# Kernel optimization log

Hardware: AMD Instinct MI355X
Metric: run time of the kernel (lower is better)

Reference implementation:

```python
import jax, jax.numpy as jnp
import numpy as np

D = 1024
H = 16
B = 4
S = 2048
NEG = -1000000000.0


def setup_inputs() -> dict:
    key = jax.random.key(0)
    ks = jax.random.split(key, 12)
    s = 0.02
    inp = {
        "Q": jax.random.normal(ks[0], (B, S, D), jnp.float32),
        "K": jax.random.normal(ks[1], (B, S, D), jnp.float32),
        "V": jax.random.normal(ks[2], (B, S, D), jnp.float32),
        # causal mask, broadcastable to [B, H, S, S]
        "mask": jnp.broadcast_to(jnp.tril(jnp.ones((S, S), bool)), (B, 1, S, S)),
        "Wq": jax.random.normal(ks[3], (D, D), jnp.float32) * s,
        "bq": jnp.zeros((D,), jnp.float32),
        "Wk": jax.random.normal(ks[4], (D, D), jnp.float32) * s,
        "bk": jnp.zeros((D,), jnp.float32),
        "Wv": jax.random.normal(ks[5], (D, D), jnp.float32) * s,
        "bv": jnp.zeros((D,), jnp.float32),
        "Wo": jax.random.normal(ks[6], (D, D), jnp.float32) * s,
        "bo": jnp.zeros((D,), jnp.float32),
    }
    return inp


def reference(Q, K, V, mask, Wq, bq, Wk, bk, Wv, bv, Wo, bo):
    d = D // H  # head dim
    def split(x):  # [B,S,D] -> [B,H,S,d]
        Bx, Sx, _ = x.shape
        return x.reshape(Bx, Sx, H, d).transpose(0, 2, 1, 3)

    q = split(Q @ Wq + bq)
    k = split(K @ Wk + bk)
    v = split(V @ Wv + bv)

    scores = jnp.einsum("bhsd,bhtd->bhst", q, k) / jnp.sqrt(jnp.float32(d))
    scores = jnp.where(mask, scores, NEG)
    attn = jax.nn.softmax(scores, axis=-1)
    out = jnp.einsum("bhst,bhtd->bhsd", attn, v)  # [B,H,S,d]
    out = out.transpose(0, 2, 1, 3).reshape(Q.shape[0], Q.shape[1], D)
    return out @ Wo + bo
```

## Files before the change

kernel.cpp:

```cpp
#include <hip/hip_runtime.h>
#include <hip/hip_bf16.h>
#include <type_traits>

#define DEV __device__ __forceinline__

typedef short bf16x8 __attribute__((ext_vector_type(8)));
typedef float f32x4 __attribute__((ext_vector_type(4)));
typedef float f32x16 __attribute__((ext_vector_type(16)));
typedef unsigned u32x4 __attribute__((ext_vector_type(4)));

static DEV unsigned short f2bf(float f) {
  unsigned u = __builtin_bit_cast(unsigned, f);
  u += 0x7FFFu + ((u >> 16) & 1u);
  return (unsigned short)(u >> 16);
}

static DEV unsigned cvtpk(float lo, float hi) {
  unsigned d;
  asm("v_cvt_pk_bf16_f32 %0, %1, %2" : "=v"(d) : "v"(lo), "v"(hi));
  return d;
}

static DEV void pl32(unsigned& x, unsigned& y) {
  asm("v_permlane32_swap_b32 %0, %1" : "+v"(x), "+v"(y));
}

static DEV void gl_lds16(const unsigned short* g, unsigned short* l) {
  __builtin_amdgcn_global_load_lds(
      (const __attribute__((address_space(1))) unsigned*)g,
      (__attribute__((address_space(3))) unsigned*)l, 16, 0, 0);
}

#define QSCALE 0.18033688f

__global__ __launch_bounds__(256) void wtrans4(const float* __restrict__ W0,
                                               const float* __restrict__ W1,
                                               const float* __restrict__ W2,
                                               const float* __restrict__ W3,
                                               unsigned short* __restrict__ T0,
                                               unsigned short* __restrict__ T1,
                                               unsigned short* __restrict__ T2,
                                               unsigned short* __restrict__ T3) {
  const int z = blockIdx.z;
  const float* W = z == 0 ? W0 : z == 1 ? W1 : z == 2 ? W2 : W3;
  unsigned short* Wt = z == 0 ? T0 : z == 1 ? T1 : z == 2 ? T2 : T3;
  const float wsc = (z == 0) ? QSCALE : 1.0f;
  __shared__ __align__(16) unsigned short T[64][72];
  const int tid = threadIdx.x;
  const int k0 = blockIdx.x * 64, n0 = blockIdx.y * 64;
  const int r = tid >> 4, c4 = (tid & 15) * 4;
  for (int j = 0; j < 4; ++j) {
    int row = j * 16 + r;
    float4 v = *(const float4*)&W[(size_t)(k0 + row) * 1024 + n0 + c4];
    ushort4 w;
    w.x = f2bf(v.x * wsc); w.y = f2bf(v.y * wsc);
    w.z = f2bf(v.z * wsc); w.w = f2bf(v.w * wsc);
    *(ushort4*)&T[row][c4] = w;
  }
  __syncthreads();
  for (int j = 0; j < 4; ++j) {
    int n = j * 16 + r;
    ushort4 w;
    w.x = T[c4 + 0][n]; w.y = T[c4 + 1][n]; w.z = T[c4 + 2][n]; w.w = T[c4 + 3][n];
    *(ushort4*)&Wt[(size_t)(n0 + n) * 1024 + k0 + c4] = w;
  }
}

template <typename InT, typename OutT, bool TRANSV>
DEV void gemm_lds_body(unsigned short* SMG, const InT* __restrict__ X,
                       const unsigned short* __restrict__ Wt,
                       const float* __restrict__ bias, OutT* __restrict__ Y,
                       float bsc) {
  unsigned short* As = SMG;
  unsigned short* Bs = SMG + 128 * 64;
  const int tid = threadIdx.x, lane = tid & 63, wid = tid >> 6;
  const int m0 = blockIdx.x * 128, n0 = blockIdx.y * 128;
  const int wm = (wid >> 1) * 64, wn = (wid & 1) * 64;
  f32x4 acc[4][4] = {};

  const int srow = wid * 32 + (lane >> 3);
  const int scol = (((lane & 7) ^ ((lane >> 3) & 7))) * 8;
  const unsigned short* gB = &Wt[(size_t)(n0 + srow) * 1024 + scol];
  unsigned short* lA = &As[wid * 32 * 64];
  unsigned short* lB = &Bs[wid * 32 * 64];

  for (int k0 = 0; k0 < 1024; k0 += 64) {
    __syncthreads();
#pragma unroll
    for (int j = 0; j < 4; ++j)
      gl_lds16(gB + (size_t)j * 8 * 1024 + k0, lB + j * 8 * 64);
    if constexpr (std::is_same_v<InT, float>) {
      const float* gAf = &X[(size_t)(m0 + srow) * 1024 + (lane & 7) * 8];
#pragma unroll
      for (int j = 0; j < 4; ++j) {
        const float* src = gAf + (size_t)j * 8 * 1024 + k0;
        float4 a0 = *(const float4*)src;
        float4 a1 = *(const float4*)(src + 4);
        uint4 w;
        w.x = cvtpk(a0.x, a0.y);
        w.y = cvtpk(a0.z, a0.w);
        w.z = cvtpk(a1.x, a1.y);
        w.w = cvtpk(a1.z, a1.w);
        *(uint4*)&As[(srow + j * 8) * 64 + scol] = w;
      }
    } else {
      const unsigned short* gA = &X[(size_t)(m0 + srow) * 1024 + scol];
#pragma unroll
      for (int j = 0; j < 4; ++j)
        gl_lds16(gA + (size_t)j * 8 * 1024 + k0, lA + j * 8 * 64);
    }
    __syncthreads();
#pragma unroll
    for (int kk = 0; kk < 2; ++kk) {
      const int kb = ((kk * 4 + (lane >> 4)) ^ (lane & 7)) * 8;
      bf16x8 af[4], bfr[4];
#pragma unroll
      for (int i = 0; i < 4; ++i)
        af[i] = *(const bf16x8*)&As[(wm + i * 16 + (lane & 15)) * 64 + kb];
#pragma unroll
      for (int i = 0; i < 4; ++i)
        bfr[i] = *(const bf16x8*)&Bs[(wn + i * 16 + (lane & 15)) * 64 + kb];
      __builtin_amdgcn_s_setprio(1);
#pragma unroll
      for (int mi = 0; mi < 4; ++mi)
#pragma unroll
        for (int ni = 0; ni < 4; ++ni)
          acc[mi][ni] =
              __builtin_amdgcn_mfma_f32_16x16x32_bf16(af[mi], bfr[ni], acc[mi][ni], 0, 0, 0);
      __builtin_amdgcn_s_setprio(0);
    }
  }

  if constexpr (TRANSV) {
    const int bt = m0 >> 11;
    const int s0 = m0 & 2047;
    const int h0 = n0 >> 6;
    unsigned short* Tl = SMG;
#pragma unroll
    for (int cch = 0; cch < 2; ++cch) {
      __syncthreads();
      if ((wid >> 1) == cch) {
#pragma unroll
        for (int ni = 0; ni < 4; ++ni) {
          const int n = wn + ni * 16 + (lane & 15);
          const float bv = bias[n0 + n] * bsc;
#pragma unroll
          for (int mi = 0; mi < 4; ++mi) {
            const int mloc = mi * 16 + (lane >> 4) * 4;
#pragma unroll
            for (int r = 0; r < 4; r += 2) {
              const unsigned pk = cvtpk(acc[mi][ni][r] + bv, acc[mi][ni][r + 1] + bv);
              *(unsigned*)&Tl[n * 72 + mloc + r] = pk;
            }
          }
        }
      }
      __syncthreads();
      const int m8 = (tid & 7) * 8;
#pragma unroll
      for (int it = 0; it < 4; ++it) {
        const int nr = (tid >> 3) + it * 32;
        const int h = h0 + (nr >> 6), dv = nr & 63;
        uint4 v = *(const uint4*)&Tl[nr * 72 + m8];
        *(uint4*)&((unsigned short*)Y)[(((size_t)bt * 16 + h) * 64 + dv) * 2048 +
                                       s0 + cch * 64 + m8] = v;
      }
    }
  } else {
    for (int ni = 0; ni < 4; ++ni) {
      const int col = n0 + wn + ni * 16 + (lane & 15);
      const float bv = bias[col] * bsc;
      for (int mi = 0; mi < 4; ++mi) {
        const int row = m0 + wm + mi * 16 + (lane >> 4) * 4;
        for (int r = 0; r < 4; ++r) {
          float v = acc[mi][ni][r] + bv;
          if constexpr (std::is_same_v<OutT, float>)
            Y[(size_t)(row + r) * 1024 + col] = v;
          else
            Y[(size_t)(row + r) * 1024 + col] = f2bf(v);
        }
      }
    }
  }
}

__global__ __launch_bounds__(256) void gemm_qkv3(
    const float* __restrict__ X0, const float* __restrict__ X1,
    const float* __restrict__ X2, const unsigned short* __restrict__ W0,
    const unsigned short* __restrict__ W1, const unsigned short* __restrict__ W2,
    const float* __restrict__ b0, const float* __restrict__ b1,
    const float* __restrict__ b2, unsigned short* __restrict__ Y0,
    unsigned short* __restrict__ Y1, unsigned short* __restrict__ Y2) {
  __shared__ __align__(16) unsigned short SMG[2 * 128 * 64];
  const int z = blockIdx.z;
  const float* X = z == 0 ? X0 : z == 1 ? X1 : X2;
  const unsigned short* Wt = z == 0 ? W0 : z == 1 ? W1 : W2;
  const float* bias = z == 0 ? b0 : z == 1 ? b1 : b2;
  unsigned short* Y = z == 0 ? Y0 : z == 1 ? Y1 : Y2;
  if (z == 2)
    gemm_lds_body<float, unsigned short, true>(SMG, X, Wt, bias, Y, 1.0f);
  else
    gemm_lds_body<float, unsigned short, false>(SMG, X, Wt, bias, Y,
                                                z == 0 ? QSCALE : 1.0f);
}

__global__ __launch_bounds__(256) void gemm_out(const unsigned short* __restrict__ X,
                                                const unsigned short* __restrict__ Wt,
                                                const float* __restrict__ bias,
                                                float* __restrict__ Y) {
  __shared__ __align__(16) unsigned short SMG[2 * 128 * 64];
  gemm_lds_body<unsigned short, float, false>(SMG, X, Wt, bias, Y, 1.0f);
}

__global__ __launch_bounds__(256) void attn_fwd(const unsigned short* __restrict__ Qb,
                                                const unsigned short* __restrict__ Kb,
                                                const unsigned short* __restrict__ Vt,
                                                unsigned short* __restrict__ Ob) {
  constexpr int KP = 72;
  __shared__ __align__(16) unsigned short SM[4 * 64 * KP];
  const int tid = threadIdx.x, lane = tid & 63, wid = tid >> 6;
  const int l31 = lane & 31, hi = lane >> 5;
  const int id = blockIdx.x;
  const int xcd = id & 7, idx = id >> 3;
  const int bh = xcd + 8 * (idx & 7);
  const int qb = idx >> 3;
  const int q0 = (15 - qb) * 128;
  const int b = bh >> 4, h = bh & 15;
  const size_t rowbase = (size_t)b * 2048;
  const int col0 = h * 64;
  const int qmin = q0 + wid * 32;
  const int myq = qmin + l31;
  const unsigned short* Vrow = Vt + (size_t)bh * 64 * 2048;
  const int rr = tid >> 3, c8 = (tid & 7) * 8;

  bf16x8 qf[4];
#pragma unroll
  for (int c = 0; c < 4; ++c)
    qf[c] = *(const bf16x8*)&Qb[(rowbase + myq) * 1024 + col0 + c * 16 + hi * 8];

  const bf16x8 onesv =
      __builtin_bit_cast(bf16x8, (u32x4){0x3F803F80u, 0x3F803F80u, 0x3F803F80u, 0x3F803F80u});

  f32x16 o[2], rsa;
  o[0] = 0.f; o[1] = 0.f; rsa = 0.f;

  const int NT = q0 / 64 + 2;
  uint4 kr0, kr1, vr0, vr1;
#define LOADT(KV0)                                                              \
  do {                                                                          \
    const int _k = (KV0);                                                       \
    kr0 = *(const uint4*)&Kb[(rowbase + _k + rr) * 1024 + col0 + c8];           \
    kr1 = *(const uint4*)&Kb[(rowbase + _k + rr + 32) * 1024 + col0 + c8];      \
    vr0 = *(const uint4*)&Vrow[(size_t)rr * 2048 + _k + c8];                    \
    vr1 = *(const uint4*)&Vrow[(size_t)(rr + 32) * 2048 + _k + c8];             \
  } while (0)

  LOADT(0);
  {
    unsigned short* Ks = SM;
    unsigned short* Vs = SM + 64 * KP;
    *(uint4*)&Ks[rr * KP + c8] = kr0;
    *(uint4*)&Ks[(rr + 32) * KP + c8] = kr1;
    *(uint4*)&Vs[rr * KP + c8] = vr0;
    *(uint4*)&Vs[(rr + 32) * KP + c8] = vr1;
    LOADT(64);
    __syncthreads();
  }

  for (int t = 0; t < NT; ++t) {
    const int kv0 = t * 64;
    const int p = t & 1;
    if (kv0 <= qmin + 31) {
      const unsigned short* Ks = SM + p * 128 * KP;
      const unsigned short* Vs = Ks + 64 * KP;

      f32x16 s2[2];
      s2[0] = 0.f; s2[1] = 0.f;
      __builtin_amdgcn_s_setprio(1);
#pragma unroll
      for (int m = 0; m < 2; ++m)
#pragma unroll
        for (int c = 0; c < 4; ++c) {
          bf16x8 kf = *(const bf16x8*)&Ks[(m * 32 + l31) * KP + c * 16 + hi * 8];
          s2[m] = __builtin_amdgcn_mfma_f32_32x32x16_bf16(kf, qf[c], s2[m], 0, 0, 0);
        }
      __builtin_amdgcn_s_setprio(0);

      if (kv0 + 63 > qmin) {
        const int thr = l31 + (qmin - kv0);
#pragma unroll
        for (int m = 0; m < 2; ++m)
#pragma unroll
          for (int r = 0; r < 16; ++r) {
            const int kvl = m * 32 + (r & 3) + 8 * (r >> 2) + 4 * hi;
            if (kvl > thr) s2[m][r] = -1.0e30f;
          }
      }

#pragma unroll
      for (int m = 0; m < 2; ++m)
#pragma unroll
        for (int r = 0; r < 16; ++r)
          s2[m][r] = __builtin_amdgcn_exp2f(s2[m][r]);

      bf16x8 pf[4];
#pragma unroll
      for (int m = 0; m < 2; ++m) {
        unsigned a0 = cvtpk(s2[m][0], s2[m][1]), a1 = cvtpk(s2[m][2], s2[m][3]);
        unsigned b0 = cvtpk(s2[m][4], s2[m][5]), b1 = cvtpk(s2[m][6], s2[m][7]);
        pl32(a0, b0);
        pl32(a1, b1);
        pf[2 * m] = __builtin_bit_cast(bf16x8, (u32x4){a0, a1, b0, b1});
        unsigned c0 = cvtpk(s2[m][8], s2[m][9]), c1 = cvtpk(s2[m][10], s2[m][11]);
        unsigned d0 = cvtpk(s2[m][12], s2[m][13]), d1 = cvtpk(s2[m][14], s2[m][15]);
        pl32(c0, d0);
        pl32(c1, d1);
        pf[2 * m + 1] = __builtin_bit_cast(bf16x8, (u32x4){c0, c1, d0, d1});
      }

      __builtin_amdgcn_s_setprio(1);
#pragma unroll
      for (int nt = 0; nt < 2; ++nt)
#pragma unroll
        for (int cc = 0; cc < 4; ++cc) {
          bf16x8 vf = *(const bf16x8*)&Vs[(nt * 32 + l31) * KP + cc * 16 + hi * 8];
          o[nt] = __builtin_amdgcn_mfma_f32_32x32x16_bf16(vf, pf[cc], o[nt], 0, 0, 0);
        }
#pragma unroll
      for (int cc = 0; cc < 4; ++cc)
        rsa = __builtin_amdgcn_mfma_f32_32x32x16_bf16(onesv, pf[cc], rsa, 0, 0, 0);
      __builtin_amdgcn_s_setprio(0);
    }
    if (t + 1 < NT) {
      unsigned short* Ks = SM + (p ^ 1) * 128 * KP;
      unsigned short* Vs = Ks + 64 * KP;
      *(uint4*)&Ks[rr * KP + c8] = kr0;
      *(uint4*)&Ks[(rr + 32) * KP + c8] = kr1;
      *(uint4*)&Vs[rr * KP + c8] = vr0;
      *(uint4*)&Vs[(rr + 32) * KP + c8] = vr1;
      if (t + 2 < NT) LOADT(kv0 + 128);
    }
    __syncthreads();
  }
#undef LOADT

  unsigned short* Os = SM + wid * 32 * KP;
  const float inv = 1.0f / rsa[0];
#pragma unroll
  for (int nt = 0; nt < 2; ++nt)
#pragma unroll
    for (int rq = 0; rq < 4; ++rq)
#pragma unroll
      for (int j = 0; j < 2; ++j) {
        const int r = rq * 4 + 2 * j;
        const unsigned pk = cvtpk(o[nt][r] * inv, o[nt][r + 1] * inv);
        *(unsigned*)&Os[l31 * KP + nt * 32 + 8 * rq + 4 * hi + 2 * j] = pk;
      }
  __syncthreads();
#pragma unroll
  for (int i = 0; i < 4; ++i) {
    const int qq = (lane >> 3) + i * 8;
    const int dvc = (lane & 7) * 8;
    uint4 val = *(const uint4*)&Os[qq * KP + dvc];
    *(uint4*)&Ob[(rowbase + qmin + qq) * 1024 + col0 + dvc] = val;
  }
}

extern "C" void kernel_launch(void* const* d_in, const int* in_sizes, int n_in,
                              void* d_out, int out_size, void* d_ws, size_t ws_size,
                              hipStream_t stream) {
  const float* Q  = (const float*)d_in[0];
  const float* K  = (const float*)d_in[1];
  const float* V  = (const float*)d_in[2];
  const float* Wq = (const float*)d_in[4];
  const float* bq = (const float*)d_in[5];
  const float* Wk = (const float*)d_in[6];
  const float* bk = (const float*)d_in[7];
  const float* Wv = (const float*)d_in[8];
  const float* bv = (const float*)d_in[9];
  const float* Wo = (const float*)d_in[10];
  const float* bo = (const float*)d_in[11];
  float* out = (float*)d_out;

  const size_t MB = 1024 * 1024;
  char* ws = (char*)d_ws;
  unsigned short* qb  = (unsigned short*)(ws + 0 * MB);
  unsigned short* kb  = (unsigned short*)(ws + 16 * MB);
  unsigned short* vtB = (unsigned short*)(ws + 32 * MB);
  unsigned short* ob  = (unsigned short*)(ws + 48 * MB);
  unsigned short* wtq = (unsigned short*)(ws + 64 * MB);
  unsigned short* wtk = (unsigned short*)(ws + 66 * MB);
  unsigned short* wtv = (unsigned short*)(ws + 68 * MB);
  unsigned short* wto = (unsigned short*)(ws + 70 * MB);

  wtrans4<<<dim3(16, 16, 4), 256, 0, stream>>>(Wq, Wk, Wv, Wo, wtq, wtk, wtv, wto);

  gemm_qkv3<<<dim3(64, 8, 3), 256, 0, stream>>>(Q, K, V, wtq, wtk, wtv,
                                                bq, bk, bv, qb, kb, vtB);

  attn_fwd<<<1024, 256, 0, stream>>>(qb, kb, vtB, ob);

  gemm_out<<<dim3(64, 8), 256, 0, stream>>>(ob, wto, bo, out);
}
```

Measured before the change: 170.5 us.

## Double-buffer GEMM LDS tiles with register prefetch and XCD-aware block remap

Restructures the shared GEMM body into a two-stage LDS ping-pong. Global-to-LDS loads and the fp32 A-tile register prefetch for the next one or two k-steps are issued before the MFMA work on the current tile, so loads overlap compute and one barrier per iteration is removed. It also remaps block ids so each XCD gets a contiguous group of M tiles, aiming at better L2 reuse. LDS per block doubles to 64KB and register pressure rises from the eight prefetched float4s, which may cut occupancy.

Measured after the change: 171.0 us. No clear change (+0.3%).

```diff
diff --git a/kernel.cpp b/kernel.cpp
--- a/kernel.cpp
+++ b/kernel.cpp
@@ -25,7 +25,7 @@
   asm("v_permlane32_swap_b32 %0, %1" : "+v"(x), "+v"(y));
 }
 
-static DEV void gl_lds16(const unsigned short* g, unsigned short* l) {
+static DEV void gl_lds16(const void* g, void* l) {
   __builtin_amdgcn_global_load_lds(
       (const __attribute__((address_space(1))) unsigned*)g,
       (__attribute__((address_space(3))) unsigned*)l, 16, 0, 0);
@@ -71,55 +71,90 @@
                        const unsigned short* __restrict__ Wt,
                        const float* __restrict__ bias, OutT* __restrict__ Y,
                        float bsc) {
-  unsigned short* As = SMG;
-  unsigned short* Bs = SMG + 128 * 64;
+  constexpr bool AF32 = std::is_same_v<InT, float>;
   const int tid = threadIdx.x, lane = tid & 63, wid = tid >> 6;
-  const int m0 = blockIdx.x * 128, n0 = blockIdx.y * 128;
+  const int id = blockIdx.y * 64 + blockIdx.x;
+  const int xcd = id & 7, jj = id >> 3;
+  const int m0 = (xcd * 8 + (jj & 7)) * 128;
+  const int n0 = (jj >> 3) * 128;
   const int wm = (wid >> 1) * 64, wn = (wid & 1) * 64;
   f32x4 acc[4][4] = {};
 
   const int srow = wid * 32 + (lane >> 3);
   const int scol = (((lane & 7) ^ ((lane >> 3) & 7))) * 8;
   const unsigned short* gB = &Wt[(size_t)(n0 + srow) * 1024 + scol];
-  unsigned short* lA = &As[wid * 32 * 64];
-  unsigned short* lB = &Bs[wid * 32 * 64];
-
-  for (int k0 = 0; k0 < 1024; k0 += 64) {
-    __syncthreads();
-#pragma unroll
-    for (int j = 0; j < 4; ++j)
-      gl_lds16(gB + (size_t)j * 8 * 1024 + k0, lB + j * 8 * 64);
-    if constexpr (std::is_same_v<InT, float>) {
-      const float* gAf = &X[(size_t)(m0 + srow) * 1024 + (lane & 7) * 8];
-#pragma unroll
-      for (int j = 0; j < 4; ++j) {
-        const float* src = gAf + (size_t)j * 8 * 1024 + k0;
-        float4 a0 = *(const float4*)src;
-        float4 a1 = *(const float4*)(src + 4);
-        uint4 w;
-        w.x = cvtpk(a0.x, a0.y);
-        w.y = cvtpk(a0.z, a0.w);
-        w.z = cvtpk(a1.x, a1.y);
-        w.w = cvtpk(a1.z, a1.w);
-        *(uint4*)&As[(srow + j * 8) * 64 + scol] = w;
-      }
-    } else {
-      const unsigned short* gA = &X[(size_t)(m0 + srow) * 1024 + scol];
-#pragma unroll
-      for (int j = 0; j < 4; ++j)
-        gl_lds16(gA + (size_t)j * 8 * 1024 + k0, lA + j * 8 * 64);
-    }
-    __syncthreads();
+  const unsigned short* gAb = nullptr;
+  const float* gAf = nullptr;
+  float4 aF[8];
+
+#define ABUF(P) (SMG + (P)*16384)
+#define BBUF(P) (SMG + (P)*16384 + 8192)
+#define DSWRITE_A(P)                                                              \
+  do {                                                                            \
+    _Pragma("unroll") for (int q = 0; q < 4; ++q) {                               \
+      uint4 w;                                                                    \
+      w.x = cvtpk(aF[2 * q].x, aF[2 * q].y);                                      \
+      w.y = cvtpk(aF[2 * q].z, aF[2 * q].w);                                      \
+      w.z = cvtpk(aF[2 * q + 1].x, aF[2 * q + 1].y);                              \
+      w.w = cvtpk(aF[2 * q + 1].z, aF[2 * q + 1].w);                              \
+      *(uint4*)&ABUF(P)[(srow + q * 8) * 64 + scol] = w;                          \
+    }                                                                             \
+  } while (0)
+#define LOAD_AF(K0)                                                               \
+  do {                                                                            \
+    _Pragma("unroll") for (int q = 0; q < 4; ++q) {                               \
+      aF[2 * q] = *(const float4*)(gAf + (size_t)q * 8192 + (K0));                \
+      aF[2 * q + 1] = *(const float4*)(gAf + (size_t)q * 8192 + (K0) + 4);        \
+    }                                                                             \
+  } while (0)
+
+  if constexpr (AF32) {
+    gAf = &X[(size_t)(m0 + srow) * 1024 + (lane & 7) * 8];
+    LOAD_AF(0);
+    DSWRITE_A(0);
+    LOAD_AF(64);
+  } else {
+    gAb = &X[(size_t)(m0 + srow) * 1024 + scol];
+#pragma unroll
+    for (int q = 0; q < 4; ++q)
+      gl_lds16(gAb + (size_t)q * 8192, &ABUF(0)[wid * 32 * 64] + q * 8 * 64);
+  }
+#pragma unroll
+  for (int q = 0; q < 4; ++q)
+    gl_lds16(gB + (size_t)q * 8192, &BBUF(0)[wid * 32 * 64] + q * 8 * 64);
+  __syncthreads();
+
+  for (int t = 0; t < 16; ++t) {
+    const int p = t & 1;
+    if (t + 1 < 16) {
+      const int kn = (t + 1) * 64;
+#pragma unroll
+      for (int q = 0; q < 4; ++q)
+        gl_lds16(gB + (size_t)q * 8192 + kn, &BBUF(p ^ 1)[wid * 32 * 64] + q * 8 * 64);
+      if constexpr (AF32) {
+        DSWRITE_A(p ^ 1);
+      } else {
+#pragma unroll
+        for (int q = 0; q < 4; ++q)
+          gl_lds16(gAb + (size_t)q * 8192 + kn, &ABUF(p ^ 1)[wid * 32 * 64] + q * 8 * 64);
+      }
+    }
+    __builtin_amdgcn_sched_barrier(0);
+    if constexpr (AF32) {
+      if (t + 2 < 16) LOAD_AF((t + 2) * 64);
+    }
+    const unsigned short* Asp = ABUF(p);
+    const unsigned short* Bsp = BBUF(p);
 #pragma unroll
     for (int kk = 0; kk < 2; ++kk) {
       const int kb = ((kk * 4 + (lane >> 4)) ^ (lane & 7)) * 8;
       bf16x8 af[4], bfr[4];
 #pragma unroll
       for (int i = 0; i < 4; ++i)
-        af[i] = *(const bf16x8*)&As[(wm + i * 16 + (lane & 15)) * 64 + kb];
+        af[i] = *(const bf16x8*)&Asp[(wm + i * 16 + (lane & 15)) * 64 + kb];
 #pragma unroll
       for (int i = 0; i < 4; ++i)
-        bfr[i] = *(const bf16x8*)&Bs[(wn + i * 16 + (lane & 15)) * 64 + kb];
+        bfr[i] = *(const bf16x8*)&Bsp[(wn + i * 16 + (lane & 15)) * 64 + kb];
       __builtin_amdgcn_s_setprio(1);
 #pragma unroll
       for (int mi = 0; mi < 4; ++mi)
@@ -129,7 +164,12 @@
               __builtin_amdgcn_mfma_f32_16x16x32_bf16(af[mi], bfr[ni], acc[mi][ni], 0, 0, 0);
       __builtin_amdgcn_s_setprio(0);
     }
-  }
+    __syncthreads();
+  }
+#undef LOAD_AF
+#undef DSWRITE_A
+#undef ABUF
+#undef BBUF
 
   if constexpr (TRANSV) {
     const int bt = m0 >> 11;
@@ -191,7 +231,7 @@
     const float* __restrict__ b0, const float* __restrict__ b1,
     const float* __restrict__ b2, unsigned short* __restrict__ Y0,
     unsigned short* __restrict__ Y1, unsigned short* __restrict__ Y2) {
-  __shared__ __align__(16) unsigned short SMG[2 * 128 * 64];
+  __shared__ __align__(16) unsigned short SMG[32768];
   const int z = blockIdx.z;
   const float* X = z == 0 ? X0 : z == 1 ? X1 : X2;
   const unsigned short* Wt = z == 0 ? W0 : z == 1 ? W1 : W2;
@@ -208,7 +248,7 @@
                                                 const unsigned short* __restrict__ Wt,
                                                 const float* __restrict__ bias,
                                                 float* __restrict__ Y) {
-  __shared__ __align__(16) unsigned short SMG[2 * 128 * 64];
+  __shared__ __align__(16) unsigned short SMG[32768];
   gemm_lds_body<unsigned short, float, false>(SMG, X, Wt, bias, Y, 1.0f);
 }
 
```
